# Kernel tuning notes

Hardware: AMD Instinct MI355X
Metric: run time of the kernel (lower is better)

Reference implementation:

```python
import jax, jax.numpy as jnp
import numpy as np

H = 128   # hidden_dim
E = 768   # embedding_dim
L = 20    # num_layers
B = 64    # batch
T = 512   # seq_len


def setup_inputs() -> dict:
    key = jax.random.key(0)
    ks = jax.random.split(key, 9)
    k = 1.0 / np.sqrt(H)  # PyTorch LSTM default init scale
    u = lambda kk, shape: jax.random.uniform(kk, shape, jnp.float32, -k, k)
    return {
        "x": jax.random.normal(ks[0], (B, T, E), jnp.float32),
        "Wih0": u(ks[1], (4 * H, E)),        # layer 0 input weights
        "Whh0": u(ks[2], (4 * H, H)),
        "bih0": u(ks[3], (4 * H,)),
        "bhh0": u(ks[4], (4 * H,)),
        "Wih": u(ks[5], (L - 1, 4 * H, H)),  # layers 1..19
        "Whh": u(ks[6], (L - 1, 4 * H, H)),
        "bih": u(ks[7], (L - 1, 4 * H)),
        "bhh": u(ks[8], (L - 1, 4 * H)),
    }


def _lstm_layer(xs, Wih, Whh, b):
    # xs: [T, B, Din] -> ys: [T, B, H], h_final: [B, H]
    bsz = xs.shape[1]
    pre = jnp.einsum('tbd,gd->tbg', xs, Wih) + b  # precompute input projections

    def step(carry, pt):
        h, c = carry
        g = pt + h @ Whh.T  # [B, 4H]
        i, f, gg, o = jnp.split(g, 4, axis=-1)  # PyTorch gate order i,f,g,o
        i = jax.nn.sigmoid(i)
        f = jax.nn.sigmoid(f)
        gg = jnp.tanh(gg)
        o = jax.nn.sigmoid(o)
        c = f * c + i * gg
        h = o * jnp.tanh(c)
        return (h, c), h

    init = (jnp.zeros((bsz, H), xs.dtype), jnp.zeros((bsz, H), xs.dtype))
    (_, _), ys = jax.lax.scan(step, init, pre)
    return ys, ys[-1]


def reference(x, Wih0, Whh0, bih0, bhh0, Wih, Whh, bih, bhh):
    xs = jnp.swapaxes(x, 0, 1)  # [T, B, E]
    ys, _ = _lstm_layer(xs, Wih0, Whh0, bih0 + bhh0)

    def layer_fn(ys, params):
        Wl, Wh, bi, bh = params
        ys2, h = _lstm_layer(ys, Wl, Wh, bi + bh)
        return ys2, h

    ys, hs = jax.lax.scan(layer_fn, ys, (Wih, Whh, bih, bhh))
    return hs[-1]  # hidden state of last (20th) layer at final timestep: [B, H]
```

## Files before the change

kernel.cpp:

```cpp
#include <hip/hip_runtime.h>

#define H4 128
#define EE 768
#define NL 20
#define TT 512
#define G4 512
#define NBG 4
#define CK 8
#define NCH (TT/CK)
#define RC 4
#define SLOT 4096
#define CHUNK (CK*SLOT)
#define FLOWB (RC*CHUNK)

typedef _Float16 v8h __attribute__((ext_vector_type(8)));
typedef _Float16 v4h __attribute__((ext_vector_type(4)));
typedef float v4f __attribute__((ext_vector_type(4)));
typedef unsigned int v4u __attribute__((ext_vector_type(4)));
typedef unsigned int v2u __attribute__((ext_vector_type(2)));

#if defined(__has_builtin)
#if __has_builtin(__builtin_amdgcn_exp2f) && __has_builtin(__builtin_amdgcn_rcpf)
#define EXP2F __builtin_amdgcn_exp2f
#define RCPF  __builtin_amdgcn_rcpf
#endif
#endif
#ifndef EXP2F
#define EXP2F exp2f
#define RCPF(x) (1.0f/(x))
#endif

__device__ __forceinline__ float fast_sig(float x) {
  float e = EXP2F(-1.44269504f * x);
  return RCPF(1.0f + e);
}
__device__ __forceinline__ float fast_tanh(float x) {
  float e = EXP2F(2.88539008f * x);
  return 1.0f - 2.0f * RCPF(1.0f + e);
}

__device__ __forceinline__ int swz(int row, int byteInRow) {
  return (row * 256 + byteInRow) ^ ((row & 15) << 4);
}

__global__ __launch_bounds__(256) void prep_kernel(
    const float* __restrict__ Wih0, const float* __restrict__ Whh0,
    const float* __restrict__ bih,  const float* __restrict__ bhh,
    const float* __restrict__ Wih,  const float* __restrict__ Whh,
    _Float16* __restrict__ W0h, _Float16* __restrict__ Wc,
    float* __restrict__ biasc, unsigned* __restrict__ flags)
{
  long idx = (long)blockIdx.x * 256 + threadIdx.x;
  const long NWC = (long)NL * G4 * 256;
  const long NW0 = (long)G4 * EE;
  const long NBI = (long)NL * G4;
  if (idx < NWC) {
    int l = (int)(idx >> 17);
    int rem = (int)(idx & 131071);
    int n = rem >> 8, kk = rem & 255;
    float v;
    if (l == 0) v = (kk < 128) ? 0.0f : Whh0[n * H4 + kk - 128];
    else v = (kk < 128) ? Wih[((long)(l-1) * G4 + n) * H4 + kk]
                        : Whh[((long)(l-1) * G4 + n) * H4 + kk - 128];
    Wc[idx] = (_Float16)v;
  } else if ((idx -= NWC) < NW0) {
    W0h[idx] = (_Float16)Wih0[idx];
  } else if ((idx -= NW0) < NBI) {
    int l = (int)(idx >> 9), n = (int)(idx & 511);
    biasc[idx] = (l == 0) ? 0.0f : (bih[(l-1) * G4 + n] + bhh[(l-1) * G4 + n]);
  } else if ((idx -= NBI) < 256) {
    flags[idx] = 0u;
  }
}

__global__ __launch_bounds__(512) void pre0_gemm(
    const float* __restrict__ x, const _Float16* __restrict__ W0h,
    const float* __restrict__ bih0, const float* __restrict__ bhh0,
    _Float16* __restrict__ pre0)
{
  __shared__ __align__(16) unsigned char smem[46080];
  _Float16* sA = (_Float16*)smem;
  _Float16* sB = (_Float16*)(smem + 5120);
  _Float16* sC = (_Float16*)smem;
  int t = blockIdx.x;
  int tid = threadIdx.x;
  int w = tid >> 6, lane = tid & 63;
  int l15 = lane & 15, kb = lane >> 4;

  v4f acc[4][4];
#pragma unroll
  for (int mi = 0; mi < 4; ++mi)
#pragma unroll
    for (int ni = 0; ni < 4; ++ni) acc[mi][ni] = (v4f){0.f, 0.f, 0.f, 0.f};

  int bA = tid >> 3, kqA = tid & 7;
  const float* xp = x + ((long)bA * TT + t) * EE + kqA * 4;
  const _Float16* wp = W0h + (long)tid * EE;

  for (int k0 = 0; k0 < EE; k0 += 32) {
    float4 xv = *(const float4*)(xp + k0);
    v4h xh = { (_Float16)xv.x, (_Float16)xv.y, (_Float16)xv.z, (_Float16)xv.w };
    *(v4h*)&sA[bA * 40 + kqA * 4] = xh;
#pragma unroll
    for (int c = 0; c < 4; ++c)
      *(v8h*)&sB[tid * 40 + c * 8] = *(const v8h*)(wp + k0 + c * 8);
    __syncthreads();
#pragma unroll
    for (int mi = 0; mi < 4; ++mi) {
      v8h a = *(const v8h*)&sA[(16 * mi + l15) * 40 + kb * 8];
#pragma unroll
      for (int ni = 0; ni < 4; ++ni) {
        v8h b = *(const v8h*)&sB[(64 * w + 16 * ni + l15) * 40 + kb * 8];
        acc[mi][ni] = __builtin_amdgcn_mfma_f32_16x16x32_f16(a, b, acc[mi][ni], 0, 0, 0);
      }
    }
    __syncthreads();
  }

#pragma unroll
  for (int hh2 = 0; hh2 < 2; ++hh2) {
    __syncthreads();
    if ((w >> 2) == hh2) {
      int wl = w & 3;
#pragma unroll
      for (int ni = 0; ni < 4; ++ni) {
        int nloc = 64 * wl + 16 * ni + l15;
        int n = 256 * hh2 + nloc;
        float bia = bih0[n] + bhh0[n];
#pragma unroll
        for (int mi = 0; mi < 4; ++mi)
#pragma unroll
          for (int r = 0; r < 4; ++r)
            sC[nloc * 72 + 16 * mi + 4 * kb + r] = (_Float16)(acc[mi][ni][r] + bia);
      }
    }
    __syncthreads();
    int row = tid >> 1, part = tid & 1;
    int n = 256 * hh2 + row;
    int n2 = (n & 127) * 4 + (n >> 7);
#pragma unroll
    for (int g = 0; g < 2; ++g) {
      int bg = part * 2 + g;
      _Float16* po = pre0 + (((long)t * NBG + bg) * 512 + n2) * 16;
      *(v8h*)po       = *(const v8h*)&sC[row * 72 + bg * 16];
      *(v8h*)(po + 8) = *(const v8h*)&sC[row * 72 + bg * 16 + 8];
    }
  }
}

__global__ __launch_bounds__(512, 1) void lstm_pipe(
    const _Float16* __restrict__ pre0, const _Float16* __restrict__ Wc,
    const float* __restrict__ biasc, _Float16* __restrict__ yring,
    unsigned* __restrict__ flags, float* __restrict__ out)
{
  __shared__ __align__(16) unsigned char lds[32768];
  const int l = blockIdx.x >> 2, bg = blockIdx.x & 3;
  const int tid = threadIdx.x, w = tid >> 6, lane = tid & 63;
  const int l15 = lane & 15, kb = lane >> 4;
  const int jloc = 16 * w + l15;

  v8h bw[4][8];
  const _Float16* wbase = Wc + (long)l * G4 * 256;
#pragma unroll
  for (int q = 0; q < 4; ++q)
#pragma unroll
    for (int ks = 0; ks < 8; ++ks)
      bw[q][ks] = *(const v8h*)(wbase + (long)(128 * q + jloc) * 256 + ks * 32 + kb * 8);

  float bias_q[4];
#pragma unroll
  for (int q = 0; q < 4; ++q)
    bias_q[q] = (l == 0) ? 0.0f : biasc[l * G4 + 128 * q + jloc];

  *(v2u*)(lds + 7 * 4096 + tid * 8) = (v2u){0u, 0u};

  const int myf = l * NBG + bg;
  const unsigned* fin  = flags + ((l > 0) ? (myf - NBG) : myf);
  const unsigned* fout = flags + ((l < NL - 1) ? (myf + NBG) : myf);
  unsigned* fme = flags + myf;
  char* ywr = (char*)yring + (long)myf * FLOWB;
  const char* yrd = (char*)yring + (long)(myf - NBG) * FLOWB;
  const char* pbase = (const char*)pre0 + (long)bg * 16384 + jloc * 128 + kb * 8;

  const int cks = tid >> 6, lane6 = tid & 63;
  const int csrc = swz(lane6 & 15, cks * 64 + (lane6 >> 4) * 16);
  const int cdst = cks * 1024 + lane6 * 16;

  v4f cst = (v4f){0.f, 0.f, 0.f, 0.f};
  v4u ya[4], yb[4];
  v2u pa[4], pb[4];

  __syncthreads();

#define ISSUE_Y(D, yslot_, ts_) do { \
    const char* a_ = (yslot_) + (long)(ts_) * SLOT + lane * 16; \
    asm volatile("global_load_dwordx4 %0, %4, off sc0 sc1\n\t" \
                 "global_load_dwordx4 %1, %4, off offset:1024 sc0 sc1\n\t" \
                 "global_load_dwordx4 %2, %4, off offset:2048 sc0 sc1\n\t" \
                 "global_load_dwordx4 %3, %4, off offset:3072 sc0 sc1" \
                 : "=v"(D[0]), "=v"(D[1]), "=v"(D[2]), "=v"(D[3]) : "v"(a_)); \
  } while (0)

#define ISSUE_P(D, t_) do { \
    const char* a_ = pbase + (long)(t_) * (NBG * 16384); \
    asm volatile("global_load_dwordx2 %0, %4, off\n\t" \
                 "global_load_dwordx2 %1, %4, off offset:32\n\t" \
                 "global_load_dwordx2 %2, %4, off offset:64\n\t" \
                 "global_load_dwordx2 %3, %4, off offset:96" \
                 : "=v"(D[0]), "=v"(D[1]), "=v"(D[2]), "=v"(D[3]) : "v"(a_)); \
  } while (0)

#define STEPX(ts_, YB, PB) do { \
    const int t = c * CK + (ts_); \
    if ((ts_) == CK - 1) asm volatile("s_waitcnt vmcnt(0)" ::: "memory"); \
    else asm volatile("s_waitcnt vmcnt(4)" ::: "memory"); \
    __builtin_amdgcn_sched_barrier(0); \
    v4f acc[4]; \
    _Pragma("unroll") \
    for (int q = 0; q < 4; ++q) \
      acc[q] = (v4f){bias_q[q], bias_q[q], bias_q[q], bias_q[q]}; \
    const unsigned char* hb = lds + (((ts_) + 7) & 7) * 4096; \
    v8h hfr[4]; \
    _Pragma("unroll") \
    for (int ks = 0; ks < 4; ++ks) \
      hfr[ks] = *(const v8h*)(hb + swz(l15, ks * 64 + kb * 16)); \
    if (l > 0) { \
      _Pragma("unroll") \
      for (int ks = 0; ks < 4; ++ks) { \
        union { v4u u; v8h h; } cv_; cv_.u = YB[ks]; \
        _Pragma("unroll") \
        for (int q = 0; q < 4; ++q) \
          acc[q] = __builtin_amdgcn_mfma_f32_16x16x32_f16(cv_.h, bw[q][ks], acc[q], 0, 0, 0); \
      } \
    } else { \
      _Pragma("unroll") \
      for (int q = 0; q < 4; ++q) { \
        union { v2u u; _Float16 h[4]; } pv_; pv_.u = PB[q]; \
        _Pragma("unroll") \
        for (int r = 0; r < 4; ++r) acc[q][r] += (float)pv_.h[r]; \
      } \
    } \
    if ((ts_) + 2 < CK) { \
      if (l > 0) ISSUE_Y(YB, yslot, (ts_) + 2); \
      else ISSUE_P(PB, t + 2); \
    } \
    _Pragma("unroll") \
    for (int ks = 0; ks < 4; ++ks) { \
      _Pragma("unroll") \
      for (int q = 0; q < 4; ++q) \
        acc[q] = __builtin_amdgcn_mfma_f32_16x16x32_f16(hfr[ks], bw[q][ks + 4], acc[q], 0, 0, 0); \
    } \
    float hf[4]; \
    _Pragma("unroll") \
    for (int r = 0; r < 4; ++r) { \
      float i_ = fast_sig(acc[0][r]); \
      float f_ = fast_sig(acc[1][r]); \
      float g_ = fast_tanh(acc[2][r]); \
      float o_ = fast_sig(acc[3][r]); \
      float cn = f_ * cst[r] + i_ * g_; \
      cst[r] = cn; \
      hf[r] = o_ * fast_tanh(cn); \
    } \
    unsigned char* hn = lds + ((ts_) & 7) * 4096; \
    _Pragma("unroll") \
    for (int r = 0; r < 4; ++r) \
      *(_Float16*)(hn + swz(4 * kb + r, jloc * 2)) = (_Float16)hf[r]; \
    if (l == NL - 1 && t == TT - 1) { \
      _Pragma("unroll") \
      for (int r = 0; r < 4; ++r) \
        out[(bg * 16 + 4 * kb + r) * H4 + jloc] = hf[r]; \
    } \
    asm volatile("s_waitcnt lgkmcnt(0)" ::: "memory"); \
    __builtin_amdgcn_s_barrier(); \
    __builtin_amdgcn_sched_barrier(0); \
  } while (0)

  for (int c = 0; c < NCH; ++c) {
    const char* yslot = yrd + (long)(c & (RC - 1)) * CHUNK;
    char* ywslot = ywr + (long)(c & (RC - 1)) * CHUNK;

    if (l > 0) {
      unsigned f;
      for (;;) {
        asm volatile("global_load_dword %0, %1, off sc0 sc1\n\ts_waitcnt vmcnt(0)"
                     : "=v"(f) : "v"(fin));
        if (f > (unsigned)c) break;
        __builtin_amdgcn_s_sleep(2);
      }
      ISSUE_Y(ya, yslot, 0);
      ISSUE_Y(yb, yslot, 1);
    } else {
      ISSUE_P(pa, c * CK);
      ISSUE_P(pb, c * CK + 1);
    }

    STEPX(0, ya, pa);
    STEPX(1, yb, pb);
    STEPX(2, ya, pa);
    STEPX(3, yb, pb);
    STEPX(4, ya, pa);
    STEPX(5, yb, pb);
    STEPX(6, ya, pa);
    STEPX(7, yb, pb);

    if (l < NL - 1) {
      if (c >= RC) {
        unsigned f;
        for (;;) {
          asm volatile("global_load_dword %0, %1, off sc0 sc1\n\ts_waitcnt vmcnt(0)"
                       : "=v"(f) : "v"(fout));
          if (f >= (unsigned)(c - RC + 1)) break;
          __builtin_amdgcn_s_sleep(2);
        }
      }
      if (tid < 256) {
#pragma unroll
        for (int ts = 0; ts < CK; ++ts) {
          v4u hv = *(const v4u*)(lds + ts * 4096 + csrc);
          asm volatile("global_store_dwordx4 %0, %1, off sc0 sc1"
                       :: "v"(ywslot + ts * 4096 + cdst), "v"(hv) : "memory");
        }
      }
    }
    asm volatile("s_waitcnt vmcnt(0)" ::: "memory");
    __builtin_amdgcn_s_barrier();
    __builtin_amdgcn_sched_barrier(0);
    if (tid == 0) {
      unsigned v = (unsigned)(c + 1);
      asm volatile("global_store_dword %0, %1, off sc0 sc1" :: "v"(fme), "v"(v) : "memory");
    }
  }
#undef STEPX
#undef ISSUE_Y
#undef ISSUE_P
}

extern "C" void kernel_launch(void* const* d_in, const int* in_sizes, int n_in,
                              void* d_out, int out_size, void* d_ws, size_t ws_size,
                              hipStream_t stream)
{
  const float* x    = (const float*)d_in[0];
  const float* Wih0 = (const float*)d_in[1];
  const float* Whh0 = (const float*)d_in[2];
  const float* bih0 = (const float*)d_in[3];
  const float* bhh0 = (const float*)d_in[4];
  const float* Wih  = (const float*)d_in[5];
  const float* Whh  = (const float*)d_in[6];
  const float* bih  = (const float*)d_in[7];
  const float* bhh  = (const float*)d_in[8];
  float* out = (float*)d_out;
  char* ws = (char*)d_ws;

  _Float16* pre0  = (_Float16*)(ws);
  _Float16* W0h   = (_Float16*)(ws + 33554432);
  _Float16* Wc    = (_Float16*)(ws + 34340864);
  float*    bc    = (float*)   (ws + 39583744);
  _Float16* yring = (_Float16*)(ws + 39624704);
  unsigned* flags = (unsigned*)(ws + 50110464);

  prep_kernel<<<11817, 256, 0, stream>>>(Wih0, Whh0, bih, bhh, Wih, Whh, W0h, Wc, bc, flags);
  pre0_gemm<<<TT, 512, 0, stream>>>(x, W0h, bih0, bhh0, pre0);
  lstm_pipe<<<NL * NBG, 512, 0, stream>>>(pre0, Wc, bc, yring, flags, out);
}
```

Measured before the change: 1.109 ms.

## Split batch into eight groups per layer, halving rows per workgroup

Raises the number of batch groups per LSTM layer from 4 to 8, so the pipeline uses 160 workgroups that each handle 8 batch rows instead of 16. The MFMA tile stays 16 rows wide, with the upper half zero-padded; lanes swap accumulator halves via shuffles so each thread computes two gate cells rather than four. This shortens the per-step elementwise work on the serial critical path. It also halves the ring depth, zeroes the y ring in the prep kernel, and changes the pre0 and ring store layouts to match. In exchange, half of the MFMA work is wasted on padding and there are more cross-workgroup flags to synchronise.

```diff
diff --git a/kernel.cpp b/kernel.cpp
--- a/kernel.cpp
+++ b/kernel.cpp
@@ -5,10 +5,10 @@
 #define NL 20
 #define TT 512
 #define G4 512
-#define NBG 4
+#define NBG 8
 #define CK 8
 #define NCH (TT/CK)
-#define RC 4
+#define RC 2
 #define SLOT 4096
 #define CHUNK (CK*SLOT)
 #define FLOWB (RC*CHUNK)
@@ -48,12 +48,14 @@
     const float* __restrict__ bih,  const float* __restrict__ bhh,
     const float* __restrict__ Wih,  const float* __restrict__ Whh,
     _Float16* __restrict__ W0h, _Float16* __restrict__ Wc,
-    float* __restrict__ biasc, unsigned* __restrict__ flags)
+    float* __restrict__ biasc, unsigned* __restrict__ flags,
+    _Float16* __restrict__ yring)
 {
   long idx = (long)blockIdx.x * 256 + threadIdx.x;
   const long NWC = (long)NL * G4 * 256;
   const long NW0 = (long)G4 * EE;
   const long NBI = (long)NL * G4;
+  const long NYR = (long)NL * NBG * FLOWB / 16;
   if (idx < NWC) {
     int l = (int)(idx >> 17);
     int rem = (int)(idx & 131071);
@@ -70,6 +72,8 @@
     biasc[idx] = (l == 0) ? 0.0f : (bih[(l-1) * G4 + n] + bhh[(l-1) * G4 + n]);
   } else if ((idx -= NBI) < 256) {
     flags[idx] = 0u;
+  } else if ((idx -= 256) < NYR) {
+    ((v4u*)yring)[idx] = (v4u){0u, 0u, 0u, 0u};
   }
 }
 
@@ -139,11 +143,10 @@
     int n = 256 * hh2 + row;
     int n2 = (n & 127) * 4 + (n >> 7);
 #pragma unroll
-    for (int g = 0; g < 2; ++g) {
-      int bg = part * 2 + g;
-      _Float16* po = pre0 + (((long)t * NBG + bg) * 512 + n2) * 16;
-      *(v8h*)po       = *(const v8h*)&sC[row * 72 + bg * 16];
-      *(v8h*)(po + 8) = *(const v8h*)&sC[row * 72 + bg * 16 + 8];
+    for (int g = 0; g < 4; ++g) {
+      int bgi = part * 4 + g;
+      _Float16* po = pre0 + (((long)t * NBG + bgi) * 512 + n2) * 8;
+      *(v8h*)po = *(const v8h*)&sC[row * 72 + bgi * 8];
     }
   }
 }
@@ -154,10 +157,12 @@
     unsigned* __restrict__ flags, float* __restrict__ out)
 {
   __shared__ __align__(16) unsigned char lds[32768];
-  const int l = blockIdx.x >> 2, bg = blockIdx.x & 3;
+  const int l = blockIdx.x >> 3, bg = blockIdx.x & 7;
   const int tid = threadIdx.x, w = tid >> 6, lane = tid & 63;
   const int l15 = lane & 15, kb = lane >> 4;
   const int jloc = 16 * w + l15;
+  const bool lo = (kb < 2);
+  const int rp = (kb & 1) * 2 + (kb >> 1);
 
   v8h bw[4][8];
   const _Float16* wbase = Wc + (long)l * G4 * 256;
@@ -172,7 +177,8 @@
   for (int q = 0; q < 4; ++q)
     bias_q[q] = (l == 0) ? 0.0f : biasc[l * G4 + 128 * q + jloc];
 
-  *(v2u*)(lds + 7 * 4096 + tid * 8) = (v2u){0u, 0u};
+  for (int i = tid; i < 2048; i += 512)
+    *(v4u*)(lds + i * 16) = (v4u){0u, 0u, 0u, 0u};
 
   const int myf = l * NBG + bg;
   const unsigned* fin  = flags + ((l > 0) ? (myf - NBG) : myf);
@@ -180,20 +186,16 @@
   unsigned* fme = flags + myf;
   char* ywr = (char*)yring + (long)myf * FLOWB;
   const char* yrd = (char*)yring + (long)(myf - NBG) * FLOWB;
-  const char* pbase = (const char*)pre0 + (long)bg * 16384 + jloc * 128 + kb * 8;
-
-  const int cks = tid >> 6, lane6 = tid & 63;
-  const int csrc = swz(lane6 & 15, cks * 64 + (lane6 >> 4) * 16);
-  const int cdst = cks * 1024 + lane6 * 16;
-
-  v4f cst = (v4f){0.f, 0.f, 0.f, 0.f};
+  const char* pbase = (const char*)pre0 + (long)bg * 8192 + jloc * 64 + kb * 8;
+
+  float c0 = 0.f, c1 = 0.f;
   v4u ya[4], yb[4];
   v2u pa[4], pb[4];
 
   __syncthreads();
 
-#define ISSUE_Y(D, yslot_, ts_) do { \
-    const char* a_ = (yslot_) + (long)(ts_) * SLOT + lane * 16; \
+#define ISSUE_Y(D, ts_) do { \
+    const char* a_ = yslot + (long)(ts_) * SLOT + lane * 16; \
     asm volatile("global_load_dwordx4 %0, %4, off sc0 sc1\n\t" \
                  "global_load_dwordx4 %1, %4, off offset:1024 sc0 sc1\n\t" \
                  "global_load_dwordx4 %2, %4, off offset:2048 sc0 sc1\n\t" \
@@ -202,11 +204,11 @@
   } while (0)
 
 #define ISSUE_P(D, t_) do { \
-    const char* a_ = pbase + (long)(t_) * (NBG * 16384); \
+    const char* a_ = pbase + (long)(t_) * (NBG * 8192); \
     asm volatile("global_load_dwordx2 %0, %4, off\n\t" \
-                 "global_load_dwordx2 %1, %4, off offset:32\n\t" \
-                 "global_load_dwordx2 %2, %4, off offset:64\n\t" \
-                 "global_load_dwordx2 %3, %4, off offset:96" \
+                 "global_load_dwordx2 %1, %4, off offset:16\n\t" \
+                 "global_load_dwordx2 %2, %4, off offset:32\n\t" \
+                 "global_load_dwordx2 %3, %4, off offset:48" \
                  : "=v"(D[0]), "=v"(D[1]), "=v"(D[2]), "=v"(D[3]) : "v"(a_)); \
   } while (0)
 
@@ -241,7 +243,7 @@
       } \
     } \
     if ((ts_) + 2 < CK) { \
-      if (l > 0) ISSUE_Y(YB, yslot, (ts_) + 2); \
+      if (l > 0) ISSUE_Y(YB, (ts_) + 2); \
       else ISSUE_P(PB, t + 2); \
     } \
     _Pragma("unroll") \
@@ -250,25 +252,29 @@
       for (int q = 0; q < 4; ++q) \
         acc[q] = __builtin_amdgcn_mfma_f32_16x16x32_f16(hfr[ks], bw[q][ks + 4], acc[q], 0, 0, 0); \
     } \
-    float hf[4]; \
+    float w0[4], w1[4]; \
     _Pragma("unroll") \
-    for (int r = 0; r < 4; ++r) { \
-      float i_ = fast_sig(acc[0][r]); \
-      float f_ = fast_sig(acc[1][r]); \
-      float g_ = fast_tanh(acc[2][r]); \
-      float o_ = fast_sig(acc[3][r]); \
-      float cn = f_ * cst[r] + i_ * g_; \
-      cst[r] = cn; \
-      hf[r] = o_ * fast_tanh(cn); \
-    } \
+    for (int q = 0; q < 4; ++q) { \
+      v4f s = acc[q]; \
+      float t2 = __shfl_xor(s[2], 32); \
+      float t3 = __shfl_xor(s[3], 32); \
+      w0[q] = lo ? s[0] : t2; \
+      w1[q] = lo ? s[1] : t3; \
+    } \
+    float i0 = fast_sig(w0[0]), f0 = fast_sig(w0[1]); \
+    float g0 = fast_tanh(w0[2]), o0 = fast_sig(w0[3]); \
+    c0 = f0 * c0 + i0 * g0; \
+    float h0 = o0 * fast_tanh(c0); \
+    float i1 = fast_sig(w1[0]), f1 = fast_sig(w1[1]); \
+    float g1 = fast_tanh(w1[2]), o1 = fast_sig(w1[3]); \
+    c1 = f1 * c1 + i1 * g1; \
+    float h1 = o1 * fast_tanh(c1); \
     unsigned char* hn = lds + ((ts_) & 7) * 4096; \
-    _Pragma("unroll") \
-    for (int r = 0; r < 4; ++r) \
-      *(_Float16*)(hn + swz(4 * kb + r, jloc * 2)) = (_Float16)hf[r]; \
+    *(_Float16*)(hn + swz(2 * rp,     jloc * 2)) = (_Float16)h0; \
+    *(_Float16*)(hn + swz(2 * rp + 1, jloc * 2)) = (_Float16)h1; \
     if (l == NL - 1 && t == TT - 1) { \
-      _Pragma("unroll") \
-      for (int r = 0; r < 4; ++r) \
-        out[(bg * 16 + 4 * kb + r) * H4 + jloc] = hf[r]; \
+      out[(bg * 8 + 2 * rp) * H4 + jloc]     = h0; \
+      out[(bg * 8 + 2 * rp + 1) * H4 + jloc] = h1; \
     } \
     asm volatile("s_waitcnt lgkmcnt(0)" ::: "memory"); \
     __builtin_amdgcn_s_barrier(); \
@@ -287,8 +293,8 @@
         if (f > (unsigned)c) break;
         __builtin_amdgcn_s_sleep(2);
       }
-      ISSUE_Y(ya, yslot, 0);
-      ISSUE_Y(yb, yslot, 1);
+      ISSUE_Y(ya, 0);
+      ISSUE_Y(yb, 1);
     } else {
       ISSUE_P(pa, c * CK);
       ISSUE_P(pb, c * CK + 1);
@@ -313,13 +319,14 @@
           __builtin_amdgcn_s_sleep(2);
         }
       }
-      if (tid < 256) {
-#pragma unroll
-        for (int ts = 0; ts < CK; ++ts) {
-          v4u hv = *(const v4u*)(lds + ts * 4096 + csrc);
-          asm volatile("global_store_dwordx4 %0, %1, off sc0 sc1"
-                       :: "v"(ywslot + ts * 4096 + cdst), "v"(hv) : "memory");
-        }
+#pragma unroll
+      for (int pass = 0; pass < 2; ++pass) {
+        const int u = tid + pass * 512;
+        const int ts2 = u >> 7, ww = u & 127, bb = ww & 7, jb = ww >> 3;
+        v4u hv = *(const v4u*)(lds + ts2 * 4096 + ((bb * 256 + jb * 16) ^ (bb << 4)));
+        char* dst2 = ywslot + ts2 * 4096 + (jb >> 2) * 1024 + (bb + 16 * (jb & 3)) * 16;
+        asm volatile("global_store_dwordx4 %0, %1, off sc0 sc1"
+                     :: "v"(dst2), "v"(hv) : "memory");
       }
     }
     asm volatile("s_waitcnt vmcnt(0)" ::: "memory");
@@ -358,7 +365,7 @@
   _Float16* yring = (_Float16*)(ws + 39624704);
   unsigned* flags = (unsigned*)(ws + 50110464);
 
-  prep_kernel<<<11817, 256, 0, stream>>>(Wih0, Whh0, bih, bhh, Wih, Whh, W0h, Wc, bc, flags);
+  prep_kernel<<<14377, 256, 0, stream>>>(Wih0, Whh0, bih, bhh, Wih, Whh, W0h, Wc, bc, flags, yring);
   pre0_gemm<<<TT, 512, 0, stream>>>(x, W0h, bih0, bhh0, pre0);
   lstm_pipe<<<NL * NBG, 512, 0, stream>>>(pre0, Wc, bc, yring, flags, out);
 }
```

After: 1.014 ms. 8.6% less time.
